# Performance work log

Measured on AMD Instinct MI355X. Metric: run time of the kernel, lower is better.

## Reference

```python
import jax, jax.numpy as jnp
import numpy as np

N, E, F_IN = 12288, 196608, 1433


def setup_inputs() -> dict:
    key = jax.random.key(0)
    ks = jax.random.split(key, 11)
    inp = {
        "x": jax.random.normal(ks[0], (N, F_IN), dtype=jnp.float32),
        "edge_index": jax.random.randint(ks[1], (2, E), 0, N, dtype=jnp.int64),
        "W1": jax.random.normal(ks[2], (F_IN, 32), dtype=jnp.float32) * 0.02,
        "b1": jnp.zeros((32,), dtype=jnp.float32),
        "Wl": jax.random.normal(ks[3], (32, 16), dtype=jnp.float32) * 0.1,
        "bl": jnp.zeros((16,), dtype=jnp.float32),
        "Wr": jax.random.normal(ks[4], (32, 16), dtype=jnp.float32) * 0.1,
        "br": jnp.zeros((16,), dtype=jnp.float32),
        "W3": jax.random.normal(ks[5], (16, 7), dtype=jnp.float32) * 0.1,
        "b3": jnp.zeros((7,), dtype=jnp.float32),
    }
    return inp


def reference(x, edge_index, W1, b1, Wl, bl, Wr, br, W3, b3):
    n = x.shape[0]
    loops = jnp.arange(n, dtype=edge_index.dtype)
    row = jnp.concatenate([edge_index[0], loops])  # [E+N]
    col = jnp.concatenate([edge_index[1], loops])

    # ---- GCN layer: dense symmetric-normalized adjacency (faithful to original) ----
    # degree computed over the col index of self-looped edges
    deg = jnp.zeros((n,), dtype=x.dtype).at[col].add(1.0)
    dis = jnp.where(deg > 0, deg ** -0.5, 0.0)  # inf -> 0 guard
    A = jnp.zeros((n, n), dtype=x.dtype).at[row, col].add(1.0)  # dense A-hat
    A_norm = dis[:, None] * A * dis[None, :]  # D^-1/2 A D^-1/2
    h = (A_norm @ x) @ W1 + b1
    h = jax.nn.relu(h)  # [N, 32]

    # ---- GraphSAGE layer: mean over neighbors j with edge (i -> j) ----
    src, dst = edge_index[0], edge_index[1]
    agg_sum = jax.ops.segment_sum(h[dst], src, num_segments=n)  # [N, 32]
    cnt = jax.ops.segment_sum(jnp.ones((src.shape[0],), dtype=h.dtype), src, num_segments=n)
    agg = jnp.where(cnt[:, None] > 0, agg_sum / jnp.maximum(cnt, 1.0)[:, None], 0.0)
    out = jax.nn.relu(h @ Wl + bl + agg @ Wr + br)  # [N, 16]
    out = out / (jnp.linalg.norm(out, axis=1, keepdims=True) + 1e-6)

    # ---- head: linear + dropout(eval: identity) + softmax ----
    logits = out @ W3 + b3  # [N, 7]
    return jax.nn.softmax(logits, axis=1)
```

## Files before the change

kernel.cpp:

```cpp
#include <hip/hip_runtime.h>
#include <hip/hip_bf16.h>
#include <math.h>

#define GN 12288
#define GE 196608
#define GK 1433
#define GC 32
#define CAP 64
#define BSTR 136
#define NSPLIT 12
#define KCHUNK 128
#define GEMMB (96 * NSPLIT)
#define EDGEB 768

typedef __attribute__((ext_vector_type(8))) short bf16x8;
typedef __attribute__((ext_vector_type(4))) float f32x4;

static __device__ inline unsigned short f2bf(float f) {
    unsigned u = __float_as_uint(f);
    unsigned r = (u + 0x7fffu + ((u >> 16) & 1u)) >> 16;
    return (unsigned short)r;
}
static __device__ inline float bf2f(unsigned short h) {
    return __uint_as_float(((unsigned)h) << 16);
}

__global__ __launch_bounds__(256) void fused_kernel(const float* __restrict__ x,
                                                    const float* __restrict__ W1,
                                                    const int* __restrict__ ei,
                                                    float* __restrict__ xw,
                                                    unsigned* __restrict__ cnt,
                                                    unsigned* __restrict__ deg,
                                                    unsigned* __restrict__ adjF) {
    int t = threadIdx.x, bid = blockIdx.x;

    if (bid >= GEMMB) {
        int e = (bid - GEMMB) * 256 + t;
        int src = ei[e];
        int dst = ei[GE + e];
        unsigned pos = atomicAdd(&cnt[src], 1u);
        if (pos < CAP) adjF[(unsigned)src * CAP + pos] = (unsigned)dst;
        atomicAdd(&deg[dst], 1u);
        return;
    }

    __shared__ unsigned short Bh[32 * BSTR], Bl[32 * BSTR];
    int lane = t & 63, w = t >> 6;
    int quad = lane >> 4, l15 = lane & 15;
    int row0 = (bid % 96) * 128;
    int ks = bid / 96;
    int k0 = ks * KCHUNK;
    int kend = min(GK, k0 + KCHUNK);
    const float* xr0 = x + (size_t)(row0 + w * 32 + l15) * GK;
    const float* xr1 = xr0 + 16 * GK;

    float a0[4][8], a1[4][8];
    #pragma unroll
    for (int it = 0; it < 4; ++it) {
        int kq = k0 + it * 32 + quad * 8;
        if (kq + 8 <= kend) {
            #pragma unroll
            for (int j = 0; j < 8; ++j) { a0[it][j] = xr0[kq + j]; a1[it][j] = xr1[kq + j]; }
        } else {
            #pragma unroll
            for (int j = 0; j < 8; ++j) {
                bool v = (kq + j) < kend;
                a0[it][j] = v ? xr0[kq + j] : 0.f;
                a1[it][j] = v ? xr1[kq + j] : 0.f;
            }
        }
    }

    #pragma unroll
    for (int e = 0; e < 16; ++e) {
        int idx = e * 256 + t;
        int kk = idx >> 5, c = idx & 31;
        int kg = k0 + kk;
        float f = (kg < kend) ? W1[(size_t)kg * GC + c] : 0.f;
        unsigned short hh = f2bf(f);
        unsigned short ll = f2bf(f - bf2f(hh));
        Bh[c * BSTR + kk] = hh;
        Bl[c * BSTR + kk] = ll;
    }
    __syncthreads();

    f32x4 acc[2][2] = {};
    #pragma unroll
    for (int it = 0; it < 4; ++it) {
        bf16x8 ah[2], al[2];
        #pragma unroll
        for (int j = 0; j < 8; ++j) {
            unsigned short h0 = f2bf(a0[it][j]);
            ah[0][j] = (short)h0; al[0][j] = (short)f2bf(a0[it][j] - bf2f(h0));
            unsigned short h1 = f2bf(a1[it][j]);
            ah[1][j] = (short)h1; al[1][j] = (short)f2bf(a1[it][j] - bf2f(h1));
        }
        bf16x8 bh[2], bl_[2];
        #pragma unroll
        for (int nt = 0; nt < 2; ++nt) {
            int c = nt * 16 + l15;
            bh[nt]  = *(bf16x8*)&Bh[c * BSTR + it * 32 + quad * 8];
            bl_[nt] = *(bf16x8*)&Bl[c * BSTR + it * 32 + quad * 8];
        }
        #pragma unroll
        for (int mt = 0; mt < 2; ++mt)
            #pragma unroll
            for (int nt = 0; nt < 2; ++nt) {
                acc[mt][nt] = __builtin_amdgcn_mfma_f32_16x16x32_bf16(ah[mt], bh[nt],  acc[mt][nt], 0, 0, 0);
                acc[mt][nt] = __builtin_amdgcn_mfma_f32_16x16x32_bf16(ah[mt], bl_[nt], acc[mt][nt], 0, 0, 0);
                acc[mt][nt] = __builtin_amdgcn_mfma_f32_16x16x32_bf16(al[mt], bh[nt],  acc[mt][nt], 0, 0, 0);
            }
    }
    #pragma unroll
    for (int mt = 0; mt < 2; ++mt)
        #pragma unroll
        for (int i = 0; i < 4; ++i) {
            int row = row0 + w * 32 + mt * 16 + quad * 4 + i;
            float* po = xw + (size_t)row * GC;
            atomicAdd(&po[l15], acc[mt][0][i]);
            atomicAdd(&po[16 + l15], acc[mt][1][i]);
        }
}

__global__ __launch_bounds__(256) void gcn_kernel(const float* __restrict__ xw,
                                                  const unsigned* __restrict__ deg,
                                                  const unsigned* __restrict__ cnt,
                                                  const unsigned* __restrict__ adjF,
                                                  const float* __restrict__ b1,
                                                  float* __restrict__ h) {
    int w = threadIdx.x >> 6;
    int lane = threadIdx.x & 63;
    int i = blockIdx.x * 4 + w;
    int f = lane & 31, half = lane >> 5;
    unsigned cl = min(cnt[i], (unsigned)CAP);
    const unsigned* ai = adjF + (unsigned)i * CAP;
    float acc = 0.f;
    for (unsigned j = half; j < cl; j += 8) {
        unsigned lim = cl - 1;
        unsigned j1 = j + 2, j2 = j + 4, j3 = j + 6;
        unsigned d0 = ai[j];
        unsigned d1 = ai[min(j1, lim)];
        unsigned d2 = ai[min(j2, lim)];
        unsigned d3 = ai[min(j3, lim)];
        float m1 = j1 < cl ? 1.f : 0.f;
        float m2 = j2 < cl ? 1.f : 0.f;
        float m3 = j3 < cl ? 1.f : 0.f;
        acc += xw[(size_t)d0 * GC + f] * rsqrtf((float)(deg[d0] + 1u));
        acc += m1 * xw[(size_t)d1 * GC + f] * rsqrtf((float)(deg[d1] + 1u));
        acc += m2 * xw[(size_t)d2 * GC + f] * rsqrtf((float)(deg[d2] + 1u));
        acc += m3 * xw[(size_t)d3 * GC + f] * rsqrtf((float)(deg[d3] + 1u));
    }
    acc += __shfl_xor(acc, 32, 64);
    float disi = rsqrtf((float)(deg[i] + 1u));
    float v = b1[f] + disi * (disi * xw[(size_t)i * GC + f] + acc);
    if (half == 0) h[(size_t)i * GC + f] = fmaxf(v, 0.f);
}

__global__ __launch_bounds__(256) void sage_kernel(const float* __restrict__ h,
                                                   const unsigned* __restrict__ cnt,
                                                   const unsigned* __restrict__ adjF,
                                                   const float* __restrict__ Wl,
                                                   const float* __restrict__ bl,
                                                   const float* __restrict__ Wr,
                                                   const float* __restrict__ br,
                                                   const float* __restrict__ W3,
                                                   const float* __restrict__ b3,
                                                   float* __restrict__ out) {
    __shared__ float sh[4][64];
    __shared__ float so[4][16];
    int w = threadIdx.x >> 6, lane = threadIdx.x & 63;
    int i = blockIdx.x * 4 + w;
    int f = lane & 31, half = lane >> 5;
    unsigned ci = cnt[i];
    unsigned cl = min(ci, (unsigned)CAP);
    const unsigned* ai = adjF + (unsigned)i * CAP;
    float acc = 0.f;
    for (unsigned j = half; j < cl; j += 8) {
        unsigned lim = cl - 1;
        unsigned j1 = j + 2, j2 = j + 4, j3 = j + 6;
        unsigned d0 = ai[j];
        unsigned d1 = ai[min(j1, lim)];
        unsigned d2 = ai[min(j2, lim)];
        unsigned d3 = ai[min(j3, lim)];
        float m1 = j1 < cl ? 1.f : 0.f;
        float m2 = j2 < cl ? 1.f : 0.f;
        float m3 = j3 < cl ? 1.f : 0.f;
        acc += h[(size_t)d0 * GC + f];
        acc += m1 * h[(size_t)d1 * GC + f];
        acc += m2 * h[(size_t)d2 * GC + f];
        acc += m3 * h[(size_t)d3 * GC + f];
    }
    acc += __shfl_xor(acc, 32, 64);
    float agg = ci ? acc / (float)ci : 0.f;
    float hv = h[(size_t)i * GC + f];
    if (half == 0) { sh[w][f] = hv; sh[w][32 + f] = agg; }
    __syncthreads();
    int c = lane;
    float hid = 0.f;
    if (c < 16) {
        hid = bl[c] + br[c];
        #pragma unroll
        for (int ff = 0; ff < 32; ++ff)
            hid += sh[w][ff] * Wl[ff * 16 + c] + sh[w][32 + ff] * Wr[ff * 16 + c];
        hid = fmaxf(hid, 0.f);
    }
    float n2 = hid * hid;
    n2 += __shfl_xor(n2, 1, 64);
    n2 += __shfl_xor(n2, 2, 64);
    n2 += __shfl_xor(n2, 4, 64);
    n2 += __shfl_xor(n2, 8, 64);
    float o = hid / (sqrtf(n2) + 1e-6f);
    if (c < 16) so[w][c] = o;
    __syncthreads();
    float logit = -INFINITY;
    if (lane < 7) {
        logit = b3[lane];
        #pragma unroll
        for (int cc = 0; cc < 16; ++cc) logit += so[w][cc] * W3[cc * 7 + lane];
    }
    float m = logit;
    m = fmaxf(m, __shfl_xor(m, 1, 64));
    m = fmaxf(m, __shfl_xor(m, 2, 64));
    m = fmaxf(m, __shfl_xor(m, 4, 64));
    float e = expf(logit - m);
    float s = e;
    s += __shfl_xor(s, 1, 64);
    s += __shfl_xor(s, 2, 64);
    s += __shfl_xor(s, 4, 64);
    if (lane < 7) out[(size_t)i * 7 + lane] = e / s;
}

extern "C" void kernel_launch(void* const* d_in, const int* in_sizes, int n_in,
                              void* d_out, int out_size, void* d_ws, size_t ws_size,
                              hipStream_t stream) {
    const float* x  = (const float*)d_in[0];
    const int*   ei = (const int*)d_in[1];
    const float* W1 = (const float*)d_in[2];
    const float* b1 = (const float*)d_in[3];
    const float* Wl = (const float*)d_in[4];
    const float* bl = (const float*)d_in[5];
    const float* Wr = (const float*)d_in[6];
    const float* br = (const float*)d_in[7];
    const float* W3 = (const float*)d_in[8];
    const float* b3 = (const float*)d_in[9];
    float* out = (float*)d_out;

    char* ws = (char*)d_ws;
    const size_t S = (size_t)GN * GC * 4;
    float*    xw   = (float*)(ws);
    unsigned* cnt  = (unsigned*)(ws + S);
    unsigned* deg  = cnt + GN;
    float*    h    = (float*)((char*)(deg + GN));
    unsigned* adjF = (unsigned*)((char*)h + S);

    hipMemsetAsync(ws, 0, S + 2 * (size_t)GN * 4, stream);
    fused_kernel<<<GEMMB + EDGEB, 256, 0, stream>>>(x, W1, ei, xw, cnt, deg, adjF);
    gcn_kernel<<<GN / 4, 256, 0, stream>>>(xw, deg, cnt, adjF, b1, h);
    sage_kernel<<<GN / 4, 256, 0, stream>>>(h, cnt, adjF, Wl, bl, Wr, br, W3, b3, out);
}
```

Baseline: 175.4 us.

## Split x bf16 hi/lo conversion into separate pass before GEMM

Adds a conversion kernel that turns x into padded bf16 hi and lo arrays, fused with the edge-adjacency build. The GEMM kernel then loads pre-split bf16 vectors directly, with K split into 9 chunks of 160. This removes per-element conversion and scalar strided loads from the GEMM, at the cost of writing and rereading an extra intermediate copy of x and one more launch.

```diff
diff --git a/kernel.cpp b/kernel.cpp
--- a/kernel.cpp
+++ b/kernel.cpp
@@ -5,12 +5,13 @@
 #define GN 12288
 #define GE 196608
 #define GK 1433
+#define GKP 1440
 #define GC 32
 #define CAP 64
-#define BSTR 136
-#define NSPLIT 12
-#define KCHUNK 128
-#define GEMMB (96 * NSPLIT)
+#define NSPLIT 9
+#define KCHUNK 160
+#define BSTR 168
+#define CONVB 3072
 #define EDGEB 768
 
 typedef __attribute__((ext_vector_type(8))) short bf16x8;
@@ -25,17 +26,16 @@
     return __uint_as_float(((unsigned)h) << 16);
 }
 
-__global__ __launch_bounds__(256) void fused_kernel(const float* __restrict__ x,
-                                                    const float* __restrict__ W1,
-                                                    const int* __restrict__ ei,
-                                                    float* __restrict__ xw,
-                                                    unsigned* __restrict__ cnt,
-                                                    unsigned* __restrict__ deg,
-                                                    unsigned* __restrict__ adjF) {
+__global__ __launch_bounds__(256) void convert_kernel(const float* __restrict__ x,
+                                                      const int* __restrict__ ei,
+                                                      unsigned short* __restrict__ xh,
+                                                      unsigned short* __restrict__ xl,
+                                                      unsigned* __restrict__ cnt,
+                                                      unsigned* __restrict__ deg,
+                                                      unsigned* __restrict__ adjF) {
     int t = threadIdx.x, bid = blockIdx.x;
-
-    if (bid >= GEMMB) {
-        int e = (bid - GEMMB) * 256 + t;
+    if (bid >= CONVB) {
+        int e = (bid - CONVB) * 256 + t;
         int src = ei[e];
         int dst = ei[GE + e];
         unsigned pos = atomicAdd(&cnt[src], 1u);
@@ -43,40 +43,54 @@
         atomicAdd(&deg[dst], 1u);
         return;
     }
-
+    int w = t >> 6, lane = t & 63;
+    int r = bid * 4 + w;
+    const float* xr = x + (size_t)r * GK;
+    unsigned short* hr = xh + (size_t)r * GKP;
+    unsigned short* lr = xl + (size_t)r * GKP;
+    #pragma unroll
+    for (int it = 0; it < 23; ++it) {
+        int k = it * 64 + lane;
+        if (k < GKP) {
+            float v = (k < GK) ? xr[k] : 0.f;
+            unsigned short h = f2bf(v);
+            unsigned short l = f2bf(v - bf2f(h));
+            hr[k] = h;
+            lr[k] = l;
+        }
+    }
+}
+
+__global__ __launch_bounds__(256) void gemm_kernel(const unsigned short* __restrict__ xh,
+                                                   const unsigned short* __restrict__ xl,
+                                                   const float* __restrict__ W1,
+                                                   float* __restrict__ xw) {
     __shared__ unsigned short Bh[32 * BSTR], Bl[32 * BSTR];
+    int t = threadIdx.x;
     int lane = t & 63, w = t >> 6;
     int quad = lane >> 4, l15 = lane & 15;
-    int row0 = (bid % 96) * 128;
-    int ks = bid / 96;
-    int k0 = ks * KCHUNK;
-    int kend = min(GK, k0 + KCHUNK);
-    const float* xr0 = x + (size_t)(row0 + w * 32 + l15) * GK;
-    const float* xr1 = xr0 + 16 * GK;
-
-    float a0[4][8], a1[4][8];
-    #pragma unroll
-    for (int it = 0; it < 4; ++it) {
+    int row0 = (blockIdx.x % 96) * 128;
+    int k0 = (blockIdx.x / 96) * KCHUNK;
+
+    size_t rbase0 = (size_t)(row0 + w * 32 + l15) * GKP;
+    size_t rbase1 = rbase0 + 16 * GKP;
+
+    bf16x8 ah0[5], al0[5], ah1[5], al1[5];
+    #pragma unroll
+    for (int it = 0; it < 5; ++it) {
         int kq = k0 + it * 32 + quad * 8;
-        if (kq + 8 <= kend) {
-            #pragma unroll
-            for (int j = 0; j < 8; ++j) { a0[it][j] = xr0[kq + j]; a1[it][j] = xr1[kq + j]; }
-        } else {
-            #pragma unroll
-            for (int j = 0; j < 8; ++j) {
-                bool v = (kq + j) < kend;
-                a0[it][j] = v ? xr0[kq + j] : 0.f;
-                a1[it][j] = v ? xr1[kq + j] : 0.f;
-            }
-        }
-    }
-
-    #pragma unroll
-    for (int e = 0; e < 16; ++e) {
+        ah0[it] = *(const bf16x8*)&xh[rbase0 + kq];
+        al0[it] = *(const bf16x8*)&xl[rbase0 + kq];
+        ah1[it] = *(const bf16x8*)&xh[rbase1 + kq];
+        al1[it] = *(const bf16x8*)&xl[rbase1 + kq];
+    }
+
+    #pragma unroll
+    for (int e = 0; e < 20; ++e) {
         int idx = e * 256 + t;
         int kk = idx >> 5, c = idx & 31;
         int kg = k0 + kk;
-        float f = (kg < kend) ? W1[(size_t)kg * GC + c] : 0.f;
+        float f = (kg < GK) ? W1[(size_t)kg * GC + c] : 0.f;
         unsigned short hh = f2bf(f);
         unsigned short ll = f2bf(f - bf2f(hh));
         Bh[c * BSTR + kk] = hh;
@@ -86,15 +100,7 @@
 
     f32x4 acc[2][2] = {};
     #pragma unroll
-    for (int it = 0; it < 4; ++it) {
-        bf16x8 ah[2], al[2];
-        #pragma unroll
-        for (int j = 0; j < 8; ++j) {
-            unsigned short h0 = f2bf(a0[it][j]);
-            ah[0][j] = (short)h0; al[0][j] = (short)f2bf(a0[it][j] - bf2f(h0));
-            unsigned short h1 = f2bf(a1[it][j]);
-            ah[1][j] = (short)h1; al[1][j] = (short)f2bf(a1[it][j] - bf2f(h1));
-        }
+    for (int it = 0; it < 5; ++it) {
         bf16x8 bh[2], bl_[2];
         #pragma unroll
         for (int nt = 0; nt < 2; ++nt) {
@@ -103,13 +109,14 @@
             bl_[nt] = *(bf16x8*)&Bl[c * BSTR + it * 32 + quad * 8];
         }
         #pragma unroll
-        for (int mt = 0; mt < 2; ++mt)
-            #pragma unroll
-            for (int nt = 0; nt < 2; ++nt) {
-                acc[mt][nt] = __builtin_amdgcn_mfma_f32_16x16x32_bf16(ah[mt], bh[nt],  acc[mt][nt], 0, 0, 0);
-                acc[mt][nt] = __builtin_amdgcn_mfma_f32_16x16x32_bf16(ah[mt], bl_[nt], acc[mt][nt], 0, 0, 0);
-                acc[mt][nt] = __builtin_amdgcn_mfma_f32_16x16x32_bf16(al[mt], bh[nt],  acc[mt][nt], 0, 0, 0);
-            }
+        for (int nt = 0; nt < 2; ++nt) {
+            acc[0][nt] = __builtin_amdgcn_mfma_f32_16x16x32_bf16(ah0[it], bh[nt],  acc[0][nt], 0, 0, 0);
+            acc[0][nt] = __builtin_amdgcn_mfma_f32_16x16x32_bf16(ah0[it], bl_[nt], acc[0][nt], 0, 0, 0);
+            acc[0][nt] = __builtin_amdgcn_mfma_f32_16x16x32_bf16(al0[it], bh[nt],  acc[0][nt], 0, 0, 0);
+            acc[1][nt] = __builtin_amdgcn_mfma_f32_16x16x32_bf16(ah1[it], bh[nt],  acc[1][nt], 0, 0, 0);
+            acc[1][nt] = __builtin_amdgcn_mfma_f32_16x16x32_bf16(ah1[it], bl_[nt], acc[1][nt], 0, 0, 0);
+            acc[1][nt] = __builtin_amdgcn_mfma_f32_16x16x32_bf16(al1[it], bh[nt],  acc[1][nt], 0, 0, 0);
+        }
     }
     #pragma unroll
     for (int mt = 0; mt < 2; ++mt)
@@ -247,14 +254,17 @@
 
     char* ws = (char*)d_ws;
     const size_t S = (size_t)GN * GC * 4;
-    float*    xw   = (float*)(ws);
-    unsigned* cnt  = (unsigned*)(ws + S);
-    unsigned* deg  = cnt + GN;
-    float*    h    = (float*)((char*)(deg + GN));
-    unsigned* adjF = (unsigned*)((char*)h + S);
+    float*          xw   = (float*)(ws);
+    unsigned*       cnt  = (unsigned*)(ws + S);
+    unsigned*       deg  = cnt + GN;
+    float*          h    = (float*)((char*)(deg + GN));
+    unsigned*       adjF = (unsigned*)((char*)h + S);
+    unsigned short* xh   = (unsigned short*)((char*)adjF + (size_t)GN * CAP * 4);
+    unsigned short* xl   = xh + (size_t)GN * GKP;
 
     hipMemsetAsync(ws, 0, S + 2 * (size_t)GN * 4, stream);
-    fused_kernel<<<GEMMB + EDGEB, 256, 0, stream>>>(x, W1, ei, xw, cnt, deg, adjF);
+    convert_kernel<<<CONVB + EDGEB, 256, 0, stream>>>(x, ei, xh, xl, cnt, deg, adjF);
+    gemm_kernel<<<96 * NSPLIT, 256, 0, stream>>>(xh, xl, W1, xw);
     gcn_kernel<<<GN / 4, 256, 0, stream>>>(xw, deg, cnt, adjF, b1, h);
     sage_kernel<<<GN / 4, 256, 0, stream>>>(h, cnt, adjF, Wl, bl, Wr, br, W3, b3, out);
 }
```

Result: slower. 195.6 us (+11.5%).

## Stage x tiles into LDS with coalesced direct global-to-LDS loads

Applied to the files above, without the earlier changes.

The GEMM part of the fused kernel previously had each lane read 8 consecutive floats of x straight into registers, spread over many rows, which coalesces poorly. It now has each wave copy whole row segments of x into an LDS tile with global_load_lds, so 64 lanes read contiguous memory. Each block now covers 64 rows instead of 128, which doubles the GEMM block count and halves the MFMA work per wave. Reads past the end of x are clamped to the last element. Past column 1433, the tail chunk picks up values from the next row, and these are cancelled by the zeroed W1 entries. The change adds 33 KB of LDS per block, which may limit occupancy.

```diff
diff --git a/kernel.cpp b/kernel.cpp
--- a/kernel.cpp
+++ b/kernel.cpp
@@ -7,10 +7,11 @@
 #define GK 1433
 #define GC 32
 #define CAP 64
-#define BSTR 136
 #define NSPLIT 12
 #define KCHUNK 128
-#define GEMMB (96 * NSPLIT)
+#define ASTR 132
+#define BSTR 136
+#define GEMMB (192 * NSPLIT)
 #define EDGEB 768
 
 typedef __attribute__((ext_vector_type(8))) short bf16x8;
@@ -23,6 +24,11 @@
 }
 static __device__ inline float bf2f(unsigned short h) {
     return __uint_as_float(((unsigned)h) << 16);
+}
+
+static __device__ inline void gload_lds4(const float* g, float* l) {
+    __builtin_amdgcn_global_load_lds((const __attribute__((address_space(1))) void*)g,
+                                     (__attribute__((address_space(3))) void*)l, 4, 0, 0);
 }
 
 __global__ __launch_bounds__(256) void fused_kernel(const float* __restrict__ x,
@@ -44,30 +50,23 @@
         return;
     }
 
+    __shared__ float As[64 * ASTR];
     __shared__ unsigned short Bh[32 * BSTR], Bl[32 * BSTR];
     int lane = t & 63, w = t >> 6;
     int quad = lane >> 4, l15 = lane & 15;
-    int row0 = (bid % 96) * 128;
-    int ks = bid / 96;
-    int k0 = ks * KCHUNK;
-    int kend = min(GK, k0 + KCHUNK);
-    const float* xr0 = x + (size_t)(row0 + w * 32 + l15) * GK;
-    const float* xr1 = xr0 + 16 * GK;
-
-    float a0[4][8], a1[4][8];
-    #pragma unroll
-    for (int it = 0; it < 4; ++it) {
-        int kq = k0 + it * 32 + quad * 8;
-        if (kq + 8 <= kend) {
-            #pragma unroll
-            for (int j = 0; j < 8; ++j) { a0[it][j] = xr0[kq + j]; a1[it][j] = xr1[kq + j]; }
-        } else {
-            #pragma unroll
-            for (int j = 0; j < 8; ++j) {
-                bool v = (kq + j) < kend;
-                a0[it][j] = v ? xr0[kq + j] : 0.f;
-                a1[it][j] = v ? xr1[kq + j] : 0.f;
-            }
+    int row0 = (bid % 192) * 64;
+    int k0 = (bid / 192) * KCHUNK;
+
+    #pragma unroll
+    for (int rr = 0; rr < 16; ++rr) {
+        int r = w * 16 + rr;
+        size_t rowbase = (size_t)(row0 + r) * GK;
+        float* lbase = &As[r * ASTR];
+        #pragma unroll
+        for (int ko = 0; ko < 2; ++ko) {
+            size_t flat = rowbase + k0 + ko * 64 + lane;
+            flat = flat < (size_t)GN * GK ? flat : (size_t)GN * GK - 1;
+            gload_lds4(x + flat, lbase + ko * 64);
         }
     }
 
@@ -76,7 +75,7 @@
         int idx = e * 256 + t;
         int kk = idx >> 5, c = idx & 31;
         int kg = k0 + kk;
-        float f = (kg < kend) ? W1[(size_t)kg * GC + c] : 0.f;
+        float f = (kg < GK) ? W1[(size_t)kg * GC + c] : 0.f;
         unsigned short hh = f2bf(f);
         unsigned short ll = f2bf(f - bf2f(hh));
         Bh[c * BSTR + kk] = hh;
@@ -84,42 +83,37 @@
     }
     __syncthreads();
 
-    f32x4 acc[2][2] = {};
+    f32x4 acc[2] = {};
     #pragma unroll
     for (int it = 0; it < 4; ++it) {
-        bf16x8 ah[2], al[2];
+        const float* ap = &As[(w * 16 + l15) * ASTR + it * 32 + quad * 8];
+        float a[8];
+        #pragma unroll
+        for (int j = 0; j < 8; ++j) a[j] = ap[j];
+        bf16x8 ah, al;
         #pragma unroll
         for (int j = 0; j < 8; ++j) {
-            unsigned short h0 = f2bf(a0[it][j]);
-            ah[0][j] = (short)h0; al[0][j] = (short)f2bf(a0[it][j] - bf2f(h0));
-            unsigned short h1 = f2bf(a1[it][j]);
-            ah[1][j] = (short)h1; al[1][j] = (short)f2bf(a1[it][j] - bf2f(h1));
+            unsigned short h0 = f2bf(a[j]);
+            ah[j] = (short)h0;
+            al[j] = (short)f2bf(a[j] - bf2f(h0));
         }
-        bf16x8 bh[2], bl_[2];
         #pragma unroll
         for (int nt = 0; nt < 2; ++nt) {
             int c = nt * 16 + l15;
-            bh[nt]  = *(bf16x8*)&Bh[c * BSTR + it * 32 + quad * 8];
-            bl_[nt] = *(bf16x8*)&Bl[c * BSTR + it * 32 + quad * 8];
+            bf16x8 bh  = *(bf16x8*)&Bh[c * BSTR + it * 32 + quad * 8];
+            bf16x8 bl_ = *(bf16x8*)&Bl[c * BSTR + it * 32 + quad * 8];
+            acc[nt] = __builtin_amdgcn_mfma_f32_16x16x32_bf16(ah, bh,  acc[nt], 0, 0, 0);
+            acc[nt] = __builtin_amdgcn_mfma_f32_16x16x32_bf16(ah, bl_, acc[nt], 0, 0, 0);
+            acc[nt] = __builtin_amdgcn_mfma_f32_16x16x32_bf16(al, bh,  acc[nt], 0, 0, 0);
         }
-        #pragma unroll
-        for (int mt = 0; mt < 2; ++mt)
-            #pragma unroll
-            for (int nt = 0; nt < 2; ++nt) {
-                acc[mt][nt] = __builtin_amdgcn_mfma_f32_16x16x32_bf16(ah[mt], bh[nt],  acc[mt][nt], 0, 0, 0);
-                acc[mt][nt] = __builtin_amdgcn_mfma_f32_16x16x32_bf16(ah[mt], bl_[nt], acc[mt][nt], 0, 0, 0);
-                acc[mt][nt] = __builtin_amdgcn_mfma_f32_16x16x32_bf16(al[mt], bh[nt],  acc[mt][nt], 0, 0, 0);
-            }
-    }
-    #pragma unroll
-    for (int mt = 0; mt < 2; ++mt)
-        #pragma unroll
-        for (int i = 0; i < 4; ++i) {
-            int row = row0 + w * 32 + mt * 16 + quad * 4 + i;
-            float* po = xw + (size_t)row * GC;
-            atomicAdd(&po[l15], acc[mt][0][i]);
-            atomicAdd(&po[16 + l15], acc[mt][1][i]);
-        }
+    }
+    #pragma unroll
+    for (int i = 0; i < 4; ++i) {
+        int row = row0 + w * 16 + quad * 4 + i;
+        float* po = xw + (size_t)row * GC;
+        atomicAdd(&po[l15], acc[0][i]);
+        atomicAdd(&po[16 + l15], acc[1][i]);
+    }
 }
 
 __global__ __launch_bounds__(256) void gcn_kernel(const float* __restrict__ xw,
```

New measurement: 176.4 us. Within noise of the previous version (+0.6%).
